# Optimization experiments

Measured on AMD Instinct MI355X. Metric: run time of the kernel, lower is better.

## Reference

```python
import jax, jax.numpy as jnp
from jax import lax
import numpy as np

T = 140
H = 64
B = 8192

def _uniform(key, shape, k):
    return jax.random.uniform(key, shape, dtype=jnp.float32, minval=-k, maxval=k)

def setup_inputs() -> dict:
    key = jax.random.key(0)
    ks = jax.random.split(key, 12)
    k = 1.0 / np.sqrt(H)  # torch default init bound
    return {
        "x": jax.random.normal(ks[0], (B, T, 1), dtype=jnp.float32),
        "h_state": jnp.zeros((2, B, H), dtype=jnp.float32),
        "W_ih0": _uniform(ks[1], (H, 1), k),
        "W_hh0": _uniform(ks[2], (H, H), k),
        "b_ih0": _uniform(ks[3], (H,), k),
        "b_hh0": _uniform(ks[4], (H,), k),
        "W_ih1": _uniform(ks[5], (H, H), k),
        "W_hh1": _uniform(ks[6], (H, H), k),
        "b_ih1": _uniform(ks[7], (H,), k),
        "b_hh1": _uniform(ks[8], (H,), k),
        "W_out": _uniform(ks[9], (1, H), k),
        "b_out": _uniform(ks[10], (1,), k),
    }

def reference(x, h_state, W_ih0, W_hh0, b_ih0, b_hh0, W_ih1, W_hh1, b_ih1, b_hh1, W_out, b_out):
    b = x.shape[0]
    x = x.reshape(b, T, 1)
    xs = jnp.swapaxes(x, 0, 1)  # [T, B, 1]

    def step(carry, xt):
        h0, h1 = carry
        # torch RNN cell: h_t = tanh(x W_ih^T + b_ih + h_{t-1} W_hh^T + b_hh)
        h0n = jnp.tanh(xt @ W_ih0.T + b_ih0 + h0 @ W_hh0.T + b_hh0)
        h1n = jnp.tanh(h0n @ W_ih1.T + b_ih1 + h1 @ W_hh1.T + b_hh1)
        return (h0n, h1n), h1n

    (hf0, hf1), ys = lax.scan(step, (h_state[0], h_state[1]), xs)
    ys = jnp.swapaxes(ys, 0, 1)  # [B, T, H]
    out = (ys @ W_out.T + b_out).reshape(b, T, 1)
    h_final = jnp.stack([hf0, hf1])  # [2, B, H]
    return out, h_final
```

## Files before the change

kernel.cpp:

```cpp
#include <hip/hip_runtime.h>

#define TT 140
#define BB 8192
#define HH 64
#define BT 16
#define HS 72
#define FP ((TT - 1) & 1)

typedef _Float16 half8 __attribute__((ext_vector_type(8)));
typedef _Float16 half4 __attribute__((ext_vector_type(4)));
typedef float    f32x4 __attribute__((ext_vector_type(4)));

#define MFMA16(a,b,c) __builtin_amdgcn_mfma_f32_16x16x32_f16(a, b, c, 0, 0, 0)

__device__ __forceinline__ float fast_tanh(float a) {
    float e = __builtin_amdgcn_exp2f(a * 2.88539008178f);
    return 1.0f - 2.0f * __builtin_amdgcn_rcpf(e + 1.0f);
}

__device__ __forceinline__ half8 ld_frag(const _Float16* p) {
    return *(const half8*)__builtin_assume_aligned(p, 16);
}

__device__ __forceinline__ half8 cvt_frag16(const float* p) {
    f32x4 wa = *(const f32x4*)p;
    f32x4 wb = *(const f32x4*)(p + 4);
    half8 h;
    #pragma unroll
    for (int j = 0; j < 8; ++j) h[j] = (_Float16)((j < 4) ? wa[j] : wb[j - 4]);
    return h;
}

__global__ __launch_bounds__(256, 2)
void rnn_kernel(const float* __restrict__ x,
                const float* __restrict__ h_state,
                const float* __restrict__ W_ih0,
                const float* __restrict__ W_hh0,
                const float* __restrict__ b_ih0,
                const float* __restrict__ b_hh0,
                const float* __restrict__ W_ih1,
                const float* __restrict__ W_hh1,
                const float* __restrict__ b_ih1,
                const float* __restrict__ b_hh1,
                const float* __restrict__ W_out,
                const float* __restrict__ b_out,
                float* __restrict__ out)
{
    __shared__ __align__(16) _Float16 h0f[2][BT * HS];
    __shared__ __align__(16) _Float16 h1f[2][BT * HS];
    __shared__ float xs[TT * 17];
    __shared__ float pps[TT * 34];

    const int tid  = threadIdx.x;
    const int w    = tid >> 6;
    const int grp  = w >> 1;
    const int wl   = w & 1;
    const int lane = tid & 63;
    const int col  = lane & 15;
    const int q    = lane >> 4;
    const int b0   = blockIdx.x * BT;

    half8 AF[2][2], AG[2][2];
    #pragma unroll
    for (int g = 0; g < 2; ++g)
    #pragma unroll
    for (int kt = 0; kt < 2; ++kt) {
        const int off = (32 * wl + 16 * g + col) * HH + 32 * kt + 8 * q;
        if (grp == 0) {
            AF[g][kt] = cvt_frag16(W_hh0 + off);
            AG[g][kt] = AF[g][kt];
        } else {
            AF[g][kt] = cvt_frag16(W_ih1 + off);
            AG[g][kt] = cvt_frag16(W_hh1 + off);
        }
    }
    float e0[2][4], e1[2][4];
    #pragma unroll
    for (int g = 0; g < 2; ++g)
    #pragma unroll
    for (int r = 0; r < 4; ++r) {
        int j = 32 * wl + 16 * g + 4 * q + r;
        if (grp == 0) { e0[g][r] = b_ih0[j] + b_hh0[j]; e1[g][r] = W_ih0[j]; }
        else          { e0[g][r] = b_ih1[j] + b_hh1[j]; e1[g][r] = W_out[j]; }
    }
    const float bout = b_out[0];

    for (int c = 0; c < (TT * BT + 255) / 256; ++c) {
        int i = c * 256 + tid;
        if (i < TT * BT) {
            int t = i >> 4, b = i & 15;
            xs[t * 17 + b] = x[(size_t)(b0 + b) * TT + t];
        }
    }
    #pragma unroll
    for (int c = 0; c < (BT * HH) / 256; ++c) {
        int i = c * 256 + tid;
        int b = i >> 6, u = i & 63;
        h0f[1][b * HS + u] = (_Float16)h_state[(size_t)(b0 + b) * HH + u];
        h1f[1][b * HS + u] = (_Float16)h_state[(size_t)BB * HH + (size_t)(b0 + b) * HH + u];
    }
    __syncthreads();

    for (int p = 0; p <= TT; ++p) {
        if (grp == 0) {
            if (p < TT) {
                const int rb = (p + 1) & 1, wb = p & 1;
                half8 Hf[2];
                #pragma unroll
                for (int kt = 0; kt < 2; ++kt)
                    Hf[kt] = ld_frag(&h0f[rb][col * HS + 32 * kt + 8 * q]);
                float xt = xs[p * 17 + col];
                #pragma unroll
                for (int g = 0; g < 2; ++g) {
                    f32x4 c = {0.f, 0.f, 0.f, 0.f};
                    c = MFMA16(AF[g][0], Hf[0], c);
                    c = MFMA16(AF[g][1], Hf[1], c);
                    half4 h4;
                    #pragma unroll
                    for (int r = 0; r < 4; ++r) {
                        float pre = c[r] + e0[g][r] + e1[g][r] * xt;
                        h4[r] = (_Float16)fast_tanh(pre);
                    }
                    *(half4*)(&h0f[wb][col * HS + 32 * wl + 16 * g + 4 * q]) = h4;
                }
            }
        } else {
            if (p >= 1) {
                const int s   = p - 1;
                const int rb0 = s & 1, rb1 = (s + 1) & 1, wb1 = s & 1;
                half8 H0f[2], H1f[2];
                #pragma unroll
                for (int kt = 0; kt < 2; ++kt) {
                    H0f[kt] = ld_frag(&h0f[rb0][col * HS + 32 * kt + 8 * q]);
                    H1f[kt] = ld_frag(&h1f[rb1][col * HS + 32 * kt + 8 * q]);
                }
                float pr = 0.f;
                #pragma unroll
                for (int g = 0; g < 2; ++g) {
                    f32x4 ci = {0.f, 0.f, 0.f, 0.f}, ch = {0.f, 0.f, 0.f, 0.f};
                    ci = MFMA16(AF[g][0], H0f[0], ci);
                    ci = MFMA16(AF[g][1], H0f[1], ci);
                    ch = MFMA16(AG[g][0], H1f[0], ch);
                    ch = MFMA16(AG[g][1], H1f[1], ch);
                    f32x4 a = ci + ch;
                    half4 h4;
                    #pragma unroll
                    for (int r = 0; r < 4; ++r) {
                        float pre = a[r] + e0[g][r];
                        float hn  = fast_tanh(pre);
                        pr += hn * e1[g][r];
                        h4[r] = (_Float16)hn;
                    }
                    *(half4*)(&h1f[wb1][col * HS + 32 * wl + 16 * g + 4 * q]) = h4;
                }
                pr += __shfl_xor(pr, 16, 64);
                pr += __shfl_xor(pr, 32, 64);
                if (lane < 16) pps[s * 34 + wl * 17 + lane] = pr;
            }
        }
        __syncthreads();
    }

    #pragma unroll
    for (int bq = 0; bq < 4; ++bq) {
        int b = 4 * bq + w;
        #pragma unroll
        for (int c = 0; c < 3; ++c) {
            int t = c * 64 + lane;
            if (t < TT)
                out[(size_t)(b0 + b) * TT + t] =
                    pps[t * 34 + b] + pps[t * 34 + 17 + b] + bout;
        }
    }
    const size_t OFF = (size_t)BB * TT;
    #pragma unroll
    for (int c = 0; c < (BT * HH) / 256; ++c) {
        int i = c * 256 + tid;
        int b = i >> 6, u = i & 63;
        out[OFF + (size_t)(b0 + b) * HH + u] = (float)h0f[FP][b * HS + u];
        out[OFF + (size_t)BB * HH + (size_t)(b0 + b) * HH + u] = (float)h1f[FP][b * HS + u];
    }
}

extern "C" void kernel_launch(void* const* d_in, const int* in_sizes, int n_in,
                              void* d_out, int out_size, void* d_ws, size_t ws_size,
                              hipStream_t stream) {
    const float* x      = (const float*)d_in[0];
    const float* hst    = (const float*)d_in[1];
    const float* W_ih0  = (const float*)d_in[2];
    const float* W_hh0  = (const float*)d_in[3];
    const float* b_ih0  = (const float*)d_in[4];
    const float* b_hh0  = (const float*)d_in[5];
    const float* W_ih1  = (const float*)d_in[6];
    const float* W_hh1  = (const float*)d_in[7];
    const float* b_ih1  = (const float*)d_in[8];
    const float* b_hh1  = (const float*)d_in[9];
    const float* W_out  = (const float*)d_in[10];
    const float* b_outp = (const float*)d_in[11];
    float* out = (float*)d_out;

    dim3 grid(BB / BT);
    dim3 block(256);
    rnn_kernel<<<grid, block, 0, stream>>>(x, hst, W_ih0, W_hh0, b_ih0, b_hh0,
                                           W_ih1, W_hh1, b_ih1, b_hh1,
                                           W_out, b_outp, out);
}
```

Before: 156.4 us.

## Split both RNN layers evenly across all four waves per step

Each wave now computes 16 hidden units of layer 0 and 16 units of layer 1 in every pipelined step. Before, two waves handled all of layer 0 and two waves handled all of layer 1, so the layer-1 waves ran twice as many MFMAs and set the critical path. The shared h0 fragments are now loaded once per wave and reused by both layers. In exchange every wave holds the fragments of all three weight matrices, and the partial-output buffer grows to four slices per timestep, which raises register and LDS use.

```diff
diff --git a/kernel.cpp b/kernel.cpp
--- a/kernel.cpp
+++ b/kernel.cpp
@@ -49,39 +49,29 @@
     __shared__ __align__(16) _Float16 h0f[2][BT * HS];
     __shared__ __align__(16) _Float16 h1f[2][BT * HS];
     __shared__ float xs[TT * 17];
-    __shared__ float pps[TT * 34];
+    __shared__ float pps[TT * 68];
 
     const int tid  = threadIdx.x;
     const int w    = tid >> 6;
-    const int grp  = w >> 1;
-    const int wl   = w & 1;
     const int lane = tid & 63;
     const int col  = lane & 15;
     const int q    = lane >> 4;
     const int b0   = blockIdx.x * BT;
 
-    half8 AF[2][2], AG[2][2];
-    #pragma unroll
-    for (int g = 0; g < 2; ++g)
+    half8 A0[2], AI[2], AH[2];
     #pragma unroll
     for (int kt = 0; kt < 2; ++kt) {
-        const int off = (32 * wl + 16 * g + col) * HH + 32 * kt + 8 * q;
-        if (grp == 0) {
-            AF[g][kt] = cvt_frag16(W_hh0 + off);
-            AG[g][kt] = AF[g][kt];
-        } else {
-            AF[g][kt] = cvt_frag16(W_ih1 + off);
-            AG[g][kt] = cvt_frag16(W_hh1 + off);
-        }
+        const int off = (16 * w + col) * HH + 32 * kt + 8 * q;
+        A0[kt] = cvt_frag16(W_hh0 + off);
+        AI[kt] = cvt_frag16(W_ih1 + off);
+        AH[kt] = cvt_frag16(W_hh1 + off);
     }
-    float e0[2][4], e1[2][4];
-    #pragma unroll
-    for (int g = 0; g < 2; ++g)
+    float e00[4], e10[4], e01[4], e11[4];
     #pragma unroll
     for (int r = 0; r < 4; ++r) {
-        int j = 32 * wl + 16 * g + 4 * q + r;
-        if (grp == 0) { e0[g][r] = b_ih0[j] + b_hh0[j]; e1[g][r] = W_ih0[j]; }
-        else          { e0[g][r] = b_ih1[j] + b_hh1[j]; e1[g][r] = W_out[j]; }
+        int j = 16 * w + 4 * q + r;
+        e00[r] = b_ih0[j] + b_hh0[j];  e10[r] = W_ih0[j];
+        e01[r] = b_ih1[j] + b_hh1[j];  e11[r] = W_out[j];
     }
     const float bout = b_out[0];
 
@@ -102,61 +92,46 @@
     __syncthreads();
 
     for (int p = 0; p <= TT; ++p) {
-        if (grp == 0) {
-            if (p < TT) {
-                const int rb = (p + 1) & 1, wb = p & 1;
-                half8 Hf[2];
-                #pragma unroll
-                for (int kt = 0; kt < 2; ++kt)
-                    Hf[kt] = ld_frag(&h0f[rb][col * HS + 32 * kt + 8 * q]);
-                float xt = xs[p * 17 + col];
-                #pragma unroll
-                for (int g = 0; g < 2; ++g) {
-                    f32x4 c = {0.f, 0.f, 0.f, 0.f};
-                    c = MFMA16(AF[g][0], Hf[0], c);
-                    c = MFMA16(AF[g][1], Hf[1], c);
-                    half4 h4;
-                    #pragma unroll
-                    for (int r = 0; r < 4; ++r) {
-                        float pre = c[r] + e0[g][r] + e1[g][r] * xt;
-                        h4[r] = (_Float16)fast_tanh(pre);
-                    }
-                    *(half4*)(&h0f[wb][col * HS + 32 * wl + 16 * g + 4 * q]) = h4;
-                }
+        const int rb = (p + 1) & 1;
+        const int wb = p & 1;
+        half8 H0a = ld_frag(&h0f[rb][col * HS + 8 * q]);
+        half8 H0b = ld_frag(&h0f[rb][col * HS + 32 + 8 * q]);
+        half8 H1a = ld_frag(&h1f[wb][col * HS + 8 * q]);
+        half8 H1b = ld_frag(&h1f[wb][col * HS + 32 + 8 * q]);
+        float xt  = xs[p * 17 + col];
+
+        if (p < TT) {
+            f32x4 c = {0.f, 0.f, 0.f, 0.f};
+            c = MFMA16(A0[0], H0a, c);
+            c = MFMA16(A0[1], H0b, c);
+            half4 h4;
+            #pragma unroll
+            for (int r = 0; r < 4; ++r) {
+                float pre = c[r] + e00[r] + e10[r] * xt;
+                h4[r] = (_Float16)fast_tanh(pre);
             }
-        } else {
-            if (p >= 1) {
-                const int s   = p - 1;
-                const int rb0 = s & 1, rb1 = (s + 1) & 1, wb1 = s & 1;
-                half8 H0f[2], H1f[2];
-                #pragma unroll
-                for (int kt = 0; kt < 2; ++kt) {
-                    H0f[kt] = ld_frag(&h0f[rb0][col * HS + 32 * kt + 8 * q]);
-                    H1f[kt] = ld_frag(&h1f[rb1][col * HS + 32 * kt + 8 * q]);
-                }
-                float pr = 0.f;
-                #pragma unroll
-                for (int g = 0; g < 2; ++g) {
-                    f32x4 ci = {0.f, 0.f, 0.f, 0.f}, ch = {0.f, 0.f, 0.f, 0.f};
-                    ci = MFMA16(AF[g][0], H0f[0], ci);
-                    ci = MFMA16(AF[g][1], H0f[1], ci);
-                    ch = MFMA16(AG[g][0], H1f[0], ch);
-                    ch = MFMA16(AG[g][1], H1f[1], ch);
-                    f32x4 a = ci + ch;
-                    half4 h4;
-                    #pragma unroll
-                    for (int r = 0; r < 4; ++r) {
-                        float pre = a[r] + e0[g][r];
-                        float hn  = fast_tanh(pre);
-                        pr += hn * e1[g][r];
-                        h4[r] = (_Float16)hn;
-                    }
-                    *(half4*)(&h1f[wb1][col * HS + 32 * wl + 16 * g + 4 * q]) = h4;
-                }
-                pr += __shfl_xor(pr, 16, 64);
-                pr += __shfl_xor(pr, 32, 64);
-                if (lane < 16) pps[s * 34 + wl * 17 + lane] = pr;
+            *(half4*)(&h0f[wb][col * HS + 16 * w + 4 * q]) = h4;
+        }
+        if (p >= 1) {
+            f32x4 ci = {0.f, 0.f, 0.f, 0.f}, ch = {0.f, 0.f, 0.f, 0.f};
+            ci = MFMA16(AI[0], H0a, ci);
+            ci = MFMA16(AI[1], H0b, ci);
+            ch = MFMA16(AH[0], H1a, ch);
+            ch = MFMA16(AH[1], H1b, ch);
+            f32x4 a = ci + ch;
+            float pr = 0.f;
+            half4 h4;
+            #pragma unroll
+            for (int r = 0; r < 4; ++r) {
+                float pre = a[r] + e01[r];
+                float hn  = fast_tanh(pre);
+                pr += hn * e11[r];
+                h4[r] = (_Float16)hn;
             }
+            *(half4*)(&h1f[rb][col * HS + 16 * w + 4 * q]) = h4;
+            pr += __shfl_xor(pr, 16, 64);
+            pr += __shfl_xor(pr, 32, 64);
+            if (lane < 16) pps[(p - 1) * 68 + w * 17 + lane] = pr;
         }
         __syncthreads();
     }
@@ -169,7 +144,8 @@
             int t = c * 64 + lane;
             if (t < TT)
                 out[(size_t)(b0 + b) * TT + t] =
-                    pps[t * 34 + b] + pps[t * 34 + 17 + b] + bout;
+                    pps[t * 68 + b] + pps[t * 68 + 17 + b]
+                  + pps[t * 68 + 34 + b] + pps[t * 68 + 51 + b] + bout;
         }
     }
     const size_t OFF = (size_t)BB * TT;
```

New measurement: 151.1 us. 1.04x faster.
